# Kernel optimization log

Measured on AMD Instinct MI355X. Metric: run time of the kernel, lower is better.

The kernel has to match this reference:

```python
import jax, jax.numpy as jnp
import numpy as np

OFFSET_SCALE = 6.0
B, H, W = 128, 256, 256


def setup_inputs() -> dict:
    key = jax.random.key(0)
    k1, k2, k3, k4 = jax.random.split(key, 4)
    Offset = jax.random.normal(k1, (B, 3, H, W), dtype=jnp.float32)
    Posmap_kpt = jax.random.normal(k2, (B, 3, H, W), dtype=jnp.float32)
    mean_posmap = jax.random.normal(k3, (3, H, W), dtype=jnp.float32)
    uv_kpt = jax.random.randint(k4, (68, 2), 0, 256, dtype=jnp.int64)
    return {"Offset": Offset, "Posmap_kpt": Posmap_kpt,
            "mean_posmap": mean_posmap, "uv_kpt": uv_kpt}


def _kpt2tform_batch(kpt_src, kpt_dst):
    # kpt_src, kpt_dst: (B, 68, 3). Index 33 is the nose-tip anchor.
    sd1 = jnp.sum(jnp.linalg.norm(kpt_src - kpt_src[:, 33:34], axis=2), axis=1)[:, None, None]
    sd2 = jnp.sum(jnp.linalg.norm(kpt_dst - kpt_dst[:, 33:34], axis=2), axis=1)[:, None, None]
    A = kpt_src * sd2 / sd1
    Bm = kpt_dst
    AA = A - A.mean(axis=1, keepdims=True)
    BB = Bm - Bm.mean(axis=1, keepdims=True)
    Hm = jnp.einsum('bki,bkj->bij', AA, BB)  # (B, 3, 3)
    U, S, Vh = jnp.linalg.svd(Hm, full_matrices=False)
    # torch.svd returns V with H = U S V^T; R = V @ U^T
    R = jnp.einsum('bji,bkj->bik', Vh, U)
    t = jnp.mean(Bm - jnp.einsum('bki,bji->bkj', A, R), axis=1)  # (B, 3)
    return R * sd2 / sd1, t


def reference(Offset, Posmap_kpt, mean_posmap, uv_kpt):
    b = Offset.shape[0]
    offsetmap = Offset * OFFSET_SCALE + mean_posmap            # (B, 3, 256, 256)
    offsetmap = jnp.transpose(offsetmap, (0, 2, 3, 1))          # (B, 256, 256, 3)
    kptmap = jnp.transpose(Posmap_kpt, (0, 2, 3, 1))
    kpt_dst = kptmap[:, uv_kpt[:, 0], uv_kpt[:, 1]]             # (B, 68, 3)
    kpt_src = offsetmap[:, uv_kpt[:, 0], uv_kpt[:, 1]]
    offs = offsetmap.reshape(b, H * W, 3)                       # (B, 65536, 3)
    R, T = _kpt2tform_batch(kpt_src, kpt_dst)
    outpos = jnp.einsum('bki,bji->bkj', offs, R) + T[:, None, :]
    outpos = outpos.reshape(b, H, W, 3)
    return jnp.transpose(outpos, (0, 3, 1, 2))
```

## Files before the change

kernel.cpp:

```cpp
#include <hip/hip_runtime.h>
#include <math.h>

#define BATCH 128
#define HH 256
#define WW 256
#define HW (HH * WW)
#define HW4 (HW / 4)
#define NKPT 68

typedef float fx4 __attribute__((ext_vector_type(4)));

__device__ inline double wave_sum64(double v) {
#pragma unroll
    for (int off = 32; off > 0; off >>= 1) v += __shfl_xor(v, off);
    return v;
}

__global__ __launch_bounds__(64, 1) void tform_kernel(
    const float* __restrict__ Offset, const float* __restrict__ Posmap,
    const float* __restrict__ meanp, const int* __restrict__ uv,
    float* __restrict__ RT) {
    const int b = blockIdx.x;
    const int lane = threadIdx.x;
    const float* offb = Offset + (size_t)b * 3 * HW;
    const float* dstb = Posmap + (size_t)b * 3 * HW;
    const bool has1 = lane < (NKPT - 64);

    double s0[3], d0[3], s1[3] = {0, 0, 0}, d1[3] = {0, 0, 0};
    {
        const int p0 = uv[lane * 2 + 0] * WW + uv[lane * 2 + 1];
#pragma unroll
        for (int i = 0; i < 3; i++) {
            s0[i] = (double)offb[(size_t)i * HW + p0] * 6.0 +
                    (double)meanp[(size_t)i * HW + p0];
            d0[i] = (double)dstb[(size_t)i * HW + p0];
        }
        if (has1) {
            const int k1 = lane + 64;
            const int p1 = uv[k1 * 2 + 0] * WW + uv[k1 * 2 + 1];
#pragma unroll
            for (int i = 0; i < 3; i++) {
                s1[i] = (double)offb[(size_t)i * HW + p1] * 6.0 +
                        (double)meanp[(size_t)i * HW + p1];
                d1[i] = (double)dstb[(size_t)i * HW + p1];
            }
        }
    }

    double s33[3], d33[3];
#pragma unroll
    for (int i = 0; i < 3; i++) {
        s33[i] = __shfl(s0[i], 33);
        d33[i] = __shfl(d0[i], 33);
    }

    double ns0 = 0, nd0 = 0, ns1 = 0, nd1 = 0;
    double ssum[3], dsum[3], P[3][3];
#pragma unroll
    for (int i = 0; i < 3; i++) {
        double es = s0[i] - s33[i], ed = d0[i] - d33[i];
        ns0 += es * es;
        nd0 += ed * ed;
        es = s1[i] - s33[i];
        ed = d1[i] - d33[i];
        ns1 += es * es;
        nd1 += ed * ed;
        ssum[i] = s0[i] + s1[i];
        dsum[i] = d0[i] + d1[i];
#pragma unroll
        for (int j = 0; j < 3; j++) P[i][j] = s0[i] * d0[j] + s1[i] * d1[j];
    }
    double sd1p = sqrt(ns0) + (has1 ? sqrt(ns1) : 0.0);
    double sd2p = sqrt(nd0) + (has1 ? sqrt(nd1) : 0.0);

    const double sd1 = wave_sum64(sd1p);
    const double sd2 = wave_sum64(sd2p);
#pragma unroll
    for (int i = 0; i < 3; i++) {
        ssum[i] = wave_sum64(ssum[i]);
        dsum[i] = wave_sum64(dsum[i]);
    }
#pragma unroll
    for (int i = 0; i < 3; i++)
#pragma unroll
        for (int j = 0; j < 3; j++) P[i][j] = wave_sum64(P[i][j]);

    if (lane != 0) return;

    const double s = sd2 / sd1;
    double sbar[3], dbar[3];
#pragma unroll
    for (int i = 0; i < 3; i++) {
        sbar[i] = ssum[i] / NKPT;
        dbar[i] = dsum[i] / NKPT;
    }

    double Hm[3][3];
    for (int i = 0; i < 3; i++)
        for (int j = 0; j < 3; j++)
            Hm[i][j] = P[i][j] - (double)NKPT * sbar[i] * dbar[j];

    double A[3][3];
    for (int i = 0; i < 3; i++)
        for (int j = 0; j < 3; j++) {
            double acc = 0;
            for (int kk = 0; kk < 3; kk++) acc += Hm[kk][i] * Hm[kk][j];
            A[i][j] = acc;
        }

    double V[3][3] = {{1, 0, 0}, {0, 1, 0}, {0, 0, 1}};
    for (int sweep = 0; sweep < 12; ++sweep) {
        double off = fabs(A[0][1]) + fabs(A[0][2]) + fabs(A[1][2]);
        double diag = fabs(A[0][0]) + fabs(A[1][1]) + fabs(A[2][2]);
        if (off <= diag * 1e-15) break;
        for (int pp = 0; pp < 2; pp++)
            for (int q = pp + 1; q < 3; q++) {
                double apq = A[pp][q];
                if (fabs(apq) < 1e-300) continue;
                double theta = (A[q][q] - A[pp][pp]) / (2.0 * apq);
                double t = (theta >= 0.0 ? 1.0 : -1.0) /
                           (fabs(theta) + sqrt(theta * theta + 1.0));
                double c = 1.0 / sqrt(t * t + 1.0);
                double sn = t * c;
                A[pp][pp] -= t * apq;
                A[q][q] += t * apq;
                A[pp][q] = 0.0;
                A[q][pp] = 0.0;
                int r = 3 - pp - q;
                double arp = A[r][pp], arq = A[r][q];
                A[r][pp] = A[pp][r] = c * arp - sn * arq;
                A[r][q] = A[q][r] = sn * arp + c * arq;
#pragma unroll
                for (int rr = 0; rr < 3; rr++) {
                    double vrp = V[rr][pp], vrq = V[rr][q];
                    V[rr][pp] = c * vrp - sn * vrq;
                    V[rr][q] = sn * vrp + c * vrq;
                }
            }
    }
    double isig[3];
#pragma unroll
    for (int i = 0; i < 3; i++) {
        double l = A[i][i];
        if (l < 1e-30) l = 1e-30;
        isig[i] = 1.0 / sqrt(l);
    }
    double Wm[3][3];
    for (int i = 0; i < 3; i++)
        for (int j = 0; j < 3; j++) {
            double acc = 0;
            for (int kk = 0; kk < 3; kk++) acc += V[i][kk] * V[j][kk] * isig[kk];
            Wm[i][j] = acc;
        }
    double R[3][3];
    for (int i = 0; i < 3; i++)
        for (int j = 0; j < 3; j++) {
            double acc = 0;
            for (int kk = 0; kk < 3; kk++) acc += Wm[i][kk] * Hm[j][kk];
            R[i][j] = acc;
        }

    float* rt = RT + b * 12;
    for (int j = 0; j < 3; j++) {
        for (int i = 0; i < 3; i++) rt[j * 3 + i] = (float)(R[j][i] * s);
        double tj = dbar[j];
        for (int i = 0; i < 3; i++) tj -= s * sbar[i] * R[j][i];
        rt[9 + j] = (float)tj;
    }
}

__global__ __launch_bounds__(256) void apply_kernel(
    const fx4* __restrict__ Off, const fx4* __restrict__ Mean,
    const float* __restrict__ RT, fx4* __restrict__ Out) {
    const int CHUNKS = HW4 / 256;
    const int b = blockIdx.x / CHUNKS;
    const int p = (blockIdx.x % CHUNKS) * 256 + threadIdx.x;

    const size_t base = (size_t)b * 3 * HW4;
    fx4 o0 = Off[base + p];
    fx4 o1 = Off[base + HW4 + p];
    fx4 o2 = Off[base + 2 * HW4 + p];
    fx4 m0 = Mean[p];
    fx4 m1 = Mean[HW4 + p];
    fx4 m2 = Mean[2 * HW4 + p];

    const float* rt = RT + b * 12;
    const float r00 = rt[0], r01 = rt[1], r02 = rt[2];
    const float r10 = rt[3], r11 = rt[4], r12 = rt[5];
    const float r20 = rt[6], r21 = rt[7], r22 = rt[8];
    const float t0 = rt[9], t1 = rt[10], t2 = rt[11];

    fx4 y0, y1, y2;
#pragma unroll
    for (int c = 0; c < 4; c++) {
        float x0 = fmaf(o0[c], 6.0f, m0[c]);
        float x1 = fmaf(o1[c], 6.0f, m1[c]);
        float x2 = fmaf(o2[c], 6.0f, m2[c]);
        y0[c] = fmaf(x0, r00, fmaf(x1, r01, fmaf(x2, r02, t0)));
        y1[c] = fmaf(x0, r10, fmaf(x1, r11, fmaf(x2, r12, t1)));
        y2[c] = fmaf(x0, r20, fmaf(x1, r21, fmaf(x2, r22, t2)));
    }

    __builtin_nontemporal_store(y0, &Out[base + p]);
    __builtin_nontemporal_store(y1, &Out[base + HW4 + p]);
    __builtin_nontemporal_store(y2, &Out[base + 2 * HW4 + p]);
}

extern "C" void kernel_launch(void* const* d_in, const int* in_sizes, int n_in,
                              void* d_out, int out_size, void* d_ws,
                              size_t ws_size, hipStream_t stream) {
    const float* Offset = (const float*)d_in[0];
    const float* Posmap = (const float*)d_in[1];
    const float* meanp = (const float*)d_in[2];
    const int* uv = (const int*)d_in[3];
    float* out = (float*)d_out;
    float* RT = (float*)d_ws;

    tform_kernel<<<BATCH, 64, 0, stream>>>(Offset, Posmap, meanp, uv, RT);
    apply_kernel<<<BATCH * (HW4 / 256), 256, 0, stream>>>(
        (const fx4*)Offset, (const fx4*)meanp, RT, (fx4*)out);
}
```

Before: 43.67 us.

## Replace Jacobi SVD with scaled Newton polar iteration; process two pixels per thread

The serial single-lane Jacobi eigendecomposition of H^T H used to build the rotation is replaced by a fixed nine-step determinant-scaled Newton iteration for the polar factor, fully unrolled and free of branches. The apply kernel now handles two float4 groups per thread and launches half as many blocks, with a launch-bounds occupancy hint added. The tform kernel is tiny, so its latency probably matters little next to the bandwidth-bound apply pass. The polar iteration also converges differently for near-singular or reflected H, which could change the result in those cases.

```diff
diff --git a/kernel.cpp b/kernel.cpp
--- a/kernel.cpp
+++ b/kernel.cpp
@@ -28,21 +28,21 @@
 
     double s0[3], d0[3], s1[3] = {0, 0, 0}, d1[3] = {0, 0, 0};
     {
-        const int p0 = uv[lane * 2 + 0] * WW + uv[lane * 2 + 1];
+        const int q0 = uv[lane * 2 + 0] * WW + uv[lane * 2 + 1];
 #pragma unroll
         for (int i = 0; i < 3; i++) {
-            s0[i] = (double)offb[(size_t)i * HW + p0] * 6.0 +
-                    (double)meanp[(size_t)i * HW + p0];
-            d0[i] = (double)dstb[(size_t)i * HW + p0];
+            s0[i] = (double)offb[(size_t)i * HW + q0] * 6.0 +
+                    (double)meanp[(size_t)i * HW + q0];
+            d0[i] = (double)dstb[(size_t)i * HW + q0];
         }
         if (has1) {
             const int k1 = lane + 64;
-            const int p1 = uv[k1 * 2 + 0] * WW + uv[k1 * 2 + 1];
+            const int q1 = uv[k1 * 2 + 0] * WW + uv[k1 * 2 + 1];
 #pragma unroll
             for (int i = 0; i < 3; i++) {
-                s1[i] = (double)offb[(size_t)i * HW + p1] * 6.0 +
-                        (double)meanp[(size_t)i * HW + p1];
-                d1[i] = (double)dstb[(size_t)i * HW + p1];
+                s1[i] = (double)offb[(size_t)i * HW + q1] * 6.0 +
+                        (double)meanp[(size_t)i * HW + q1];
+                d1[i] = (double)dstb[(size_t)i * HW + q1];
             }
         }
     }
@@ -94,95 +94,75 @@
         sbar[i] = ssum[i] / NKPT;
         dbar[i] = dsum[i] / NKPT;
     }
-
     double Hm[3][3];
+#pragma unroll
     for (int i = 0; i < 3; i++)
+#pragma unroll
         for (int j = 0; j < 3; j++)
             Hm[i][j] = P[i][j] - (double)NKPT * sbar[i] * dbar[j];
 
-    double A[3][3];
+    double X[3][3];
+#pragma unroll
     for (int i = 0; i < 3; i++)
-        for (int j = 0; j < 3; j++) {
-            double acc = 0;
-            for (int kk = 0; kk < 3; kk++) acc += Hm[kk][i] * Hm[kk][j];
-            A[i][j] = acc;
-        }
-
-    double V[3][3] = {{1, 0, 0}, {0, 1, 0}, {0, 0, 1}};
-    for (int sweep = 0; sweep < 12; ++sweep) {
-        double off = fabs(A[0][1]) + fabs(A[0][2]) + fabs(A[1][2]);
-        double diag = fabs(A[0][0]) + fabs(A[1][1]) + fabs(A[2][2]);
-        if (off <= diag * 1e-15) break;
-        for (int pp = 0; pp < 2; pp++)
-            for (int q = pp + 1; q < 3; q++) {
-                double apq = A[pp][q];
-                if (fabs(apq) < 1e-300) continue;
-                double theta = (A[q][q] - A[pp][pp]) / (2.0 * apq);
-                double t = (theta >= 0.0 ? 1.0 : -1.0) /
-                           (fabs(theta) + sqrt(theta * theta + 1.0));
-                double c = 1.0 / sqrt(t * t + 1.0);
-                double sn = t * c;
-                A[pp][pp] -= t * apq;
-                A[q][q] += t * apq;
-                A[pp][q] = 0.0;
-                A[q][pp] = 0.0;
-                int r = 3 - pp - q;
-                double arp = A[r][pp], arq = A[r][q];
-                A[r][pp] = A[pp][r] = c * arp - sn * arq;
-                A[r][q] = A[q][r] = sn * arp + c * arq;
-#pragma unroll
-                for (int rr = 0; rr < 3; rr++) {
-                    double vrp = V[rr][pp], vrq = V[rr][q];
-                    V[rr][pp] = c * vrp - sn * vrq;
-                    V[rr][q] = sn * vrp + c * vrq;
-                }
-            }
-    }
-    double isig[3];
-#pragma unroll
-    for (int i = 0; i < 3; i++) {
-        double l = A[i][i];
-        if (l < 1e-30) l = 1e-30;
-        isig[i] = 1.0 / sqrt(l);
-    }
-    double Wm[3][3];
-    for (int i = 0; i < 3; i++)
-        for (int j = 0; j < 3; j++) {
-            double acc = 0;
-            for (int kk = 0; kk < 3; kk++) acc += V[i][kk] * V[j][kk] * isig[kk];
-            Wm[i][j] = acc;
-        }
-    double R[3][3];
-    for (int i = 0; i < 3; i++)
-        for (int j = 0; j < 3; j++) {
-            double acc = 0;
-            for (int kk = 0; kk < 3; kk++) acc += Wm[i][kk] * Hm[j][kk];
-            R[i][j] = acc;
-        }
+#pragma unroll
+        for (int j = 0; j < 3; j++) X[i][j] = Hm[j][i];
+
+#pragma unroll
+    for (int it = 0; it < 9; ++it) {
+        double C[3][3];
+        C[0][0] = X[1][1] * X[2][2] - X[1][2] * X[2][1];
+        C[0][1] = X[1][2] * X[2][0] - X[1][0] * X[2][2];
+        C[0][2] = X[1][0] * X[2][1] - X[1][1] * X[2][0];
+        C[1][0] = X[0][2] * X[2][1] - X[0][1] * X[2][2];
+        C[1][1] = X[0][0] * X[2][2] - X[0][2] * X[2][0];
+        C[1][2] = X[0][1] * X[2][0] - X[0][0] * X[2][1];
+        C[2][0] = X[0][1] * X[1][2] - X[0][2] * X[1][1];
+        C[2][1] = X[0][2] * X[1][0] - X[0][0] * X[1][2];
+        C[2][2] = X[0][0] * X[1][1] - X[0][1] * X[1][0];
+        double det =
+            X[0][0] * C[0][0] + X[0][1] * C[0][1] + X[0][2] * C[0][2];
+        double ad = fabs(det);
+        if (ad < 1e-250) ad = 1e-250;
+        const double mu = 1.0 / cbrt(ad);
+        const double inv = 1.0 / (mu * det);
+#pragma unroll
+        for (int i = 0; i < 3; i++)
+#pragma unroll
+            for (int j = 0; j < 3; j++)
+                X[i][j] = 0.5 * (mu * X[i][j] + C[i][j] * inv);
+    }
 
     float* rt = RT + b * 12;
     for (int j = 0; j < 3; j++) {
-        for (int i = 0; i < 3; i++) rt[j * 3 + i] = (float)(R[j][i] * s);
+        for (int i = 0; i < 3; i++) rt[j * 3 + i] = (float)(X[j][i] * s);
         double tj = dbar[j];
-        for (int i = 0; i < 3; i++) tj -= s * sbar[i] * R[j][i];
+        for (int i = 0; i < 3; i++) tj -= s * sbar[i] * X[j][i];
         rt[9 + j] = (float)tj;
     }
 }
 
-__global__ __launch_bounds__(256) void apply_kernel(
+__global__ __launch_bounds__(256, 4) void apply_kernel(
     const fx4* __restrict__ Off, const fx4* __restrict__ Mean,
     const float* __restrict__ RT, fx4* __restrict__ Out) {
-    const int CHUNKS = HW4 / 256;
-    const int b = blockIdx.x / CHUNKS;
-    const int p = (blockIdx.x % CHUNKS) * 256 + threadIdx.x;
-
+    const int PAIRS = HW4 / 512;
+    const int b = blockIdx.x / PAIRS;
+    const int w = blockIdx.x % PAIRS;
+    const int p0 = w * 512 + threadIdx.x;
+    const int p1 = p0 + 256;
     const size_t base = (size_t)b * 3 * HW4;
-    fx4 o0 = Off[base + p];
-    fx4 o1 = Off[base + HW4 + p];
-    fx4 o2 = Off[base + 2 * HW4 + p];
-    fx4 m0 = Mean[p];
-    fx4 m1 = Mean[HW4 + p];
-    fx4 m2 = Mean[2 * HW4 + p];
+
+    fx4 a0 = Off[base + p0];
+    fx4 a1 = Off[base + HW4 + p0];
+    fx4 a2 = Off[base + 2 * HW4 + p0];
+    fx4 b0 = Off[base + p1];
+    fx4 b1 = Off[base + HW4 + p1];
+    fx4 b2 = Off[base + 2 * HW4 + p1];
+    fx4 ma0 = Mean[p0];
+    fx4 ma1 = Mean[HW4 + p0];
+    fx4 ma2 = Mean[2 * HW4 + p0];
+    fx4 mb0 = Mean[p1];
+    fx4 mb1 = Mean[HW4 + p1];
+    fx4 mb2 = Mean[2 * HW4 + p1];
 
     const float* rt = RT + b * 12;
     const float r00 = rt[0], r01 = rt[1], r02 = rt[2];
@@ -190,20 +170,29 @@
     const float r20 = rt[6], r21 = rt[7], r22 = rt[8];
     const float t0 = rt[9], t1 = rt[10], t2 = rt[11];
 
-    fx4 y0, y1, y2;
-#pragma unroll
-    for (int c = 0; c < 4; c++) {
-        float x0 = fmaf(o0[c], 6.0f, m0[c]);
-        float x1 = fmaf(o1[c], 6.0f, m1[c]);
-        float x2 = fmaf(o2[c], 6.0f, m2[c]);
-        y0[c] = fmaf(x0, r00, fmaf(x1, r01, fmaf(x2, r02, t0)));
-        y1[c] = fmaf(x0, r10, fmaf(x1, r11, fmaf(x2, r12, t1)));
-        y2[c] = fmaf(x0, r20, fmaf(x1, r21, fmaf(x2, r22, t2)));
-    }
-
-    __builtin_nontemporal_store(y0, &Out[base + p]);
-    __builtin_nontemporal_store(y1, &Out[base + HW4 + p]);
-    __builtin_nontemporal_store(y2, &Out[base + 2 * HW4 + p]);
+    fx4 y0, y1, y2, z0, z1, z2;
+#pragma unroll
+    for (int e = 0; e < 4; e++) {
+        float x0 = fmaf(a0[e], 6.0f, ma0[e]);
+        float x1 = fmaf(a1[e], 6.0f, ma1[e]);
+        float x2 = fmaf(a2[e], 6.0f, ma2[e]);
+        y0[e] = fmaf(x0, r00, fmaf(x1, r01, fmaf(x2, r02, t0)));
+        y1[e] = fmaf(x0, r10, fmaf(x1, r11, fmaf(x2, r12, t1)));
+        y2[e] = fmaf(x0, r20, fmaf(x1, r21, fmaf(x2, r22, t2)));
+        float u0 = fmaf(b0[e], 6.0f, mb0[e]);
+        float u1 = fmaf(b1[e], 6.0f, mb1[e]);
+        float u2 = fmaf(b2[e], 6.0f, mb2[e]);
+        z0[e] = fmaf(u0, r00, fmaf(u1, r01, fmaf(u2, r02, t0)));
+        z1[e] = fmaf(u0, r10, fmaf(u1, r11, fmaf(u2, r12, t1)));
+        z2[e] = fmaf(u0, r20, fmaf(u1, r21, fmaf(u2, r22, t2)));
+    }
+
+    __builtin_nontemporal_store(y0, &Out[base + p0]);
+    __builtin_nontemporal_store(y1, &Out[base + HW4 + p0]);
+    __builtin_nontemporal_store(y2, &Out[base + 2 * HW4 + p0]);
+    __builtin_nontemporal_store(z0, &Out[base + p1]);
+    __builtin_nontemporal_store(z1, &Out[base + HW4 + p1]);
+    __builtin_nontemporal_store(z2, &Out[base + 2 * HW4 + p1]);
 }
 
 extern "C" void kernel_launch(void* const* d_in, const int* in_sizes, int n_in,
@@ -217,6 +206,6 @@
     float* RT = (float*)d_ws;
 
     tform_kernel<<<BATCH, 64, 0, stream>>>(Offset, Posmap, meanp, uv, RT);
-    apply_kernel<<<BATCH * (HW4 / 256), 256, 0, stream>>>(
+    apply_kernel<<<BATCH * (HW4 / 512), 256, 0, stream>>>(
         (const fx4*)Offset, (const fx4*)meanp, RT, (fx4*)out);
 }
```

Measured after the change: 41.72 us. -4.5%, faster.
